# Optimization experiments

Measured on AMD Instinct MI355X. Metric: run time of the kernel, lower is better.

The kernel has to match this reference:

```python
import jax, jax.numpy as jnp
import numpy as np

L, N, E, D, H, B = 4, 50000, 800000, 128, 64, 16384
ED = 2 * D  # edge_dim
K = 7      # conv1d kernel size


def setup_inputs() -> dict:
    key = jax.random.key(0)
    ks = jax.random.split(key, 12)
    return {
        "x_nodes": jax.random.normal(ks[0], (L, N, 1), jnp.float32),
        "edge_index": jax.random.randint(ks[1], (L, 2, E), 0, N),
        "W1": jax.random.normal(ks[2], (L, 1, H), jnp.float32) * 0.1,
        "b1": jnp.zeros((L, H), jnp.float32),
        "gamma": jnp.ones((L, H), jnp.float32),
        "beta": jnp.zeros((L, H), jnp.float32),
        "W2": jax.random.normal(ks[3], (L, H, D), jnp.float32) * 0.05,
        "b2": jnp.zeros((L, D), jnp.float32),
        "conv_w": jax.random.normal(ks[4], (ED, ED, K), jnp.float32) * 0.02,
        "conv_b": jnp.zeros((ED,), jnp.float32),
        "lc_w": jax.random.normal(ks[5], (ED, L), jnp.float32) * 0.05,
        "lc_b": jnp.zeros((L,), jnp.float32),
        "link_w": jax.random.normal(ks[6], (ED, 2), jnp.float32) * 0.05,
        "link_b": jnp.zeros((2,), jnp.float32),
        "now_layer": jax.random.randint(ks[7], (B,), 0, L),
        "leftnode": jax.random.randint(ks[8], (B,), 0, N),
        "rightnode": jax.random.randint(ks[9], (B,), 0, N),
    }


def gcn_conv(x, src, dst, norm, W, b):
    # x: [N, Fin] -> [N, Fout]; symmetric-normalized message passing (GCNConv)
    xw = x @ W
    out = jax.ops.segment_sum(norm[:, None] * xw[src], dst, num_segments=N)
    return out + b


def gcn_layer(x, ei, W1, b1, g, bt, W2, b2):
    loops = jnp.arange(N, dtype=ei.dtype)
    src = jnp.concatenate([ei[0], loops])
    dst = jnp.concatenate([ei[1], loops])
    deg = jax.ops.segment_sum(jnp.ones_like(src, jnp.float32), dst, num_segments=N)
    dis = jax.lax.rsqrt(jnp.maximum(deg, 1e-12))
    norm = dis[src] * dis[dst]
    h = gcn_conv(x, src, dst, norm, W1, b1)
    # BatchNorm1d (training mode: batch stats over nodes)
    mu = h.mean(axis=0)
    var = h.var(axis=0)
    h = g * (h - mu) * jax.lax.rsqrt(var + 1e-5) + bt
    h = jax.nn.relu(h)
    return gcn_conv(h, src, dst, norm, W2, b2)


def reference(x_nodes, edge_index, W1, b1, gamma, beta, W2, b2,
              conv_w, conv_b, lc_w, lc_b, link_w, link_b,
              now_layer, leftnode, rightnode):
    # Per-layer GCN embeddings (fixed small L -> Python loop is fine, keeps peak memory low)
    embeds = jnp.stack([
        gcn_layer(x_nodes[i], edge_index[i], W1[i], b1[i], gamma[i], beta[i], W2[i], b2[i])
        for i in range(L)
    ])  # [L, N, D]

    # Edge features: gather per-sample layer-specific node embeddings and concat
    left = embeds[now_layer, leftnode]    # [B, D]
    right = embeds[now_layer, rightnode]  # [B, D]
    layer_specific = jnp.concatenate([left, right], axis=-1)  # [B, ED]

    # Conv1d applied unbatched on [ED, B] (convolves across batch dim, as in original)
    dn = jax.lax.conv_dimension_numbers((1, ED, B), (ED, ED, K), ('NCH', 'OIH', 'NCH'))
    y = jax.lax.conv_general_dilated(layer_specific.T[None], conv_w, (1,), [(3, 3)],
                                     dimension_numbers=dn)[0]  # [ED, B]
    shared = jax.nn.relu(y + conv_b[:, None]).T  # [B, ED]

    discriminant_outs = shared @ lc_w + lc_b  # [B, L]

    # Ortho_algorithm: remove shared component from specific, combine with shared
    dot = jnp.sum(layer_specific * shared, axis=-1, keepdims=True)
    nrm = jnp.sum(shared * shared, axis=-1, keepdims=True)
    enhanced = layer_specific - (dot / (nrm + 1e-12)) * shared + shared  # [B, ED]

    prediction_outs = enhanced @ link_w + link_b  # [B, 2]
    return prediction_outs, discriminant_outs
```

## Files before the change

kernel.cpp:

```cpp
#include <hip/hip_runtime.h>
#include <hip/hip_bf16.h>

#define Lc 4
#define Nc 50000
#define Ec 800000
#define Bc 16384
#define EDc 256
#define Kc 7
#define Mtot (Lc * Nc)
#define KDIM (EDc * Kc)

#define BINW 512
#define BSH 9
#define FB 98
#define NBINS (FB * Lc)
#define CAPc 12288
#define CHUNK 8192
#define FBLK ((Ec + CHUNK - 1) / CHUNK)

#define PADTOT 33024
#define PADBIT (1 << 24)

typedef __attribute__((ext_vector_type(8))) short bf16x8;
typedef __attribute__((ext_vector_type(4))) float f32x4;

static __device__ __forceinline__ unsigned short f2bf(float f) {
    unsigned u = __float_as_uint(f);
    unsigned r = (u + 0x7fffu + ((u >> 16) & 1u)) >> 16;
    return (unsigned short)r;
}
static __device__ __forceinline__ float bf2f(unsigned short u) {
    return __uint_as_float(((unsigned)u) << 16);
}


__global__ __launch_bounds__(1024) void k_binfill(const int* __restrict__ ei,
                                                  int* __restrict__ binCursor,
                                                  int* __restrict__ binned) {
    int l = blockIdx.y;
    int e0 = blockIdx.x * CHUNK;
    __shared__ int lh[FB], lcur[FB];
    if (threadIdx.x < FB) lh[threadIdx.x] = 0;
    __syncthreads();
    const int* srcp = ei + (size_t)l * 2 * Ec;
    const int* dstp = srcp + Ec;
#pragma unroll
    for (int it = 0; it < CHUNK / 1024; it++) {
        int idx = e0 + it * 1024 + threadIdx.x;
        if (idx < Ec) atomicAdd(&lh[dstp[idx] >> BSH], 1);
    }
    __syncthreads();
    if (threadIdx.x < FB) {
        int c = lh[threadIdx.x];
        int bin = l * FB + threadIdx.x;
        int st = c ? atomicAdd(&binCursor[bin], c) : 0;
        lcur[threadIdx.x] = bin * CAPc + min(st, CAPc);
        lh[threadIdx.x] = bin * CAPc + CAPc;
    }
    __syncthreads();
#pragma unroll
    for (int it = 0; it < CHUNK / 1024; it++) {
        int idx = e0 + it * 1024 + threadIdx.x;
        if (idx < Ec) {
            int d = dstp[idx], sv = srcp[idx];
            int t = d >> BSH;
            int pos = atomicAdd(&lcur[t], 1);
            if (pos < lh[t]) binned[pos] = (sv << BSH) | (d & (BINW - 1));
        }
    }
}

__global__ void k_mark(const int* __restrict__ now, const int* __restrict__ lnn,
                       const int* __restrict__ rnn, int* __restrict__ ord,
                       unsigned* __restrict__ bitmap, int* __restrict__ gcnt) {
    int b = blockIdx.x * 256 + threadIdx.x;
    for (int p = b; p < PADTOT; p += 16384) ord[p] = PADBIT;
    int l = now[b];
    int a1 = l * Nc + lnn[b];
    atomicOr(&bitmap[a1 >> 5], 1u << (a1 & 31));
    int a2 = l * Nc + rnn[b];
    atomicOr(&bitmap[a2 >> 5], 1u << (a2 & 31));
    int lane = threadIdx.x & 63;
#pragma unroll
    for (int ll = 0; ll < 4; ll++) {
        unsigned long long m = __ballot(l == ll);
        if (m && lane == __builtin_ctzll(m)) atomicAdd(&gcnt[ll], __popcll(m));
    }
}

__global__ void k_order2(const int* __restrict__ now, const int* __restrict__ gcnt,
                         int* __restrict__ gcur, int* __restrict__ ord) {
    int b = blockIdx.x * 256 + threadIdx.x;
    int l = now[b];
    int segBase = 0;
    for (int ll = 0; ll < l; ll++) segBase += (2 * gcnt[ll] + 63) & ~63;
    int lane = threadIdx.x & 63;
#pragma unroll
    for (int ll = 0; ll < 4; ll++) {
        unsigned long long m = __ballot(l == ll);
        if (!m) continue;
        int ldr = __builtin_ctzll(m);
        int bs = 0;
        if (lane == ldr) bs = atomicAdd(&gcur[ll], __popcll(m));
        bs = __shfl(bs, ldr);
        if (l == ll) {
            int rk = __popcll(m & (lane ? ((1ull << lane) - 1) : 0ull));
            int sp = segBase + 2 * (bs + rk);
            ord[sp] = (2 * b) | (ll << 20);
            ord[sp + 1] = (2 * b + 1) | (ll << 20);
        }
    }
}

__global__ __launch_bounds__(512) void k_csr(const int* __restrict__ binCnt,
                                             const int* __restrict__ binned,
                                             const float* __restrict__ x_nodes,
                                             const unsigned* __restrict__ bitmap,
                                             int* __restrict__ csr,
                                             int* __restrict__ rstart,
                                             int* __restrict__ cnt,
                                             float* __restrict__ dis,
                                             float* __restrict__ g) {
    int b = blockIdx.x;
    int l = b / FB, gg = b % FB;
    int rs = b * CAPc;
    int cntb = binCnt[b];
    if (cntb > CAPc) cntb = CAPc;
    int re = rs + cntb;
    __shared__ int hist[BINW];
    hist[threadIdx.x] = 0;
    __syncthreads();
    for (int i = rs + threadIdx.x; i < re; i += 512)
        atomicAdd(&hist[binned[i] & (BINW - 1)], 1);
    __syncthreads();
    int lane = threadIdx.x & 63, wid = threadIdx.x >> 6;
    int v = hist[threadIdx.x];
    int x = v;
#pragma unroll
    for (int off = 1; off < 64; off <<= 1) {
        int y = __shfl_up(x, off);
        if (lane >= off) x += y;
    }
    __shared__ int ws[8];
    if (lane == 63) ws[wid] = x;
    __syncthreads();
    int carry = 0;
    for (int w = 0; w < wid; w++) carry += ws[w];
    int exc = x - v + carry;
    int n = gg * BINW + threadIdx.x;
    int n4 = l * Nc + n;
    if (n < Nc) {
        rstart[n4] = rs + exc;
        cnt[n4] = v;
        float dn = rsqrtf((float)v + 1.0f);
        dis[n4] = dn;
        g[n4] = dn * x_nodes[(size_t)l * Nc + n];
    }
    __syncthreads();
    hist[threadIdx.x] = rs + exc;
    __syncthreads();
    int lbase = l * Nc + gg * BINW;
    for (int i = rs + threadIdx.x; i < re; i += 512) {
        unsigned p = (unsigned)binned[i];
        int d = p & (BINW - 1);
        int nn4 = lbase + d;
        if ((bitmap[nn4 >> 5] >> (nn4 & 31)) & 1u) {
            int pos = atomicAdd(&hist[d], 1);
            csr[pos] = (int)(p >> BSH);
        }
    }
}

__global__ __launch_bounds__(512) void k_s_bin(const int* __restrict__ binCnt,
                                               const int* __restrict__ binned,
                                               const float* __restrict__ g,
                                               const float* __restrict__ dis,
                                               float2* __restrict__ ns,
                                               double* __restrict__ stats) {
    int b = blockIdx.x;
    int l = b / FB, gg = b % FB;
    int rs = b * CAPc;
    int cntb = binCnt[b];
    if (cntb > CAPc) cntb = CAPc;
    int re = rs + cntb;
    const float* gl = g + (size_t)l * Nc;
    __shared__ float acc[BINW];
    acc[threadIdx.x] = 0.f;
    __syncthreads();
    for (int i = rs + threadIdx.x; i < re; i += 512) {
        unsigned p = (unsigned)binned[i];
        atomicAdd(&acc[p & (BINW - 1)], gl[p >> BSH]);
    }
    __syncthreads();
    int n = gg * BINW + threadIdx.x;
    int n4 = l * Nc + n;
    double v = 0.0, v2 = 0.0;
    if (n < Nc) {
        float dn = dis[n4];
        float sf = dn * (acc[threadIdx.x] + g[n4]);
        ns[n4] = make_float2(dn, sf);
        v = (double)sf;
        v2 = (double)sf * (double)sf;
    }
    for (int m = 32; m; m >>= 1) { v += __shfl_xor(v, m); v2 += __shfl_xor(v2, m); }
    __shared__ double r0[8], r1[8];
    int wid = threadIdx.x >> 6, lane = threadIdx.x & 63;
    if (lane == 0) { r0[wid] = v; r1[wid] = v2; }
    __syncthreads();
    if (threadIdx.x == 0) {
        double a = 0, bb = 0;
        for (int w = 0; w < 8; w++) { a += r0[w]; bb += r1[w]; }
        atomicAdd(&stats[l * 2 + 0], a);
        atomicAdd(&stats[l * 2 + 1], bb);
    }
}

__global__ void k_cvec4(const double* __restrict__ stats, const float* __restrict__ W1,
                        const float* __restrict__ gamma, float* __restrict__ cbuf) {
    int l = threadIdx.x >> 6, h = threadIdx.x & 63;
    double mean = stats[l * 2] / (double)Nc;
    double var = stats[l * 2 + 1] / (double)Nc - mean * mean;
    float w = W1[l * 64 + h];
    cbuf[l * 72 + h] = gamma[l * 64 + h] * w * rsqrtf((float)var * w * w + 1e-5f);
    if (h == 0) cbuf[l * 72 + 64] = (float)mean;
}


__global__ __launch_bounds__(256) void k_agg(const int* __restrict__ ord,
        const int* __restrict__ lnn, const int* __restrict__ rnn,
        const int* __restrict__ rstart, const int* __restrict__ cnt,
        const int* __restrict__ csr, const float2* __restrict__ ns,
        const float* __restrict__ cbuf, const float* __restrict__ beta,
        unsigned short* __restrict__ acch) {
    int pos = blockIdx.x * 4 + (threadIdx.x >> 6);
    int lane = threadIdx.x & 63;
    int ordv = ord[pos];
    if (ordv & PADBIT) { acch[(size_t)pos * 64 + lane] = 0; return; }
    int side = ordv & 0xFFFFF;
    int l = (ordv >> 20) & 3;
    int b = side >> 1;
    int n = (side & 1) ? rnn[b] : lnn[b];
    int n4 = l * Nc + n;
    float c = cbuf[l * 72 + lane], mu = cbuf[l * 72 + 64], bt = beta[l * 64 + lane];
    const float2* nsl = ns + (size_t)l * Nc;
    int st = rstart[n4], deg = cnt[n4];
    float a = 0.f;
    for (int base = 0; base < deg; base += 64) {
        int e = base + lane;
        int sv = (e < deg) ? csr[st + e] : 0;
        float nv = 0.f, fv = 0.f;
        if (e < deg) {
            float2 nf = nsl[sv];
            nv = nf.x; fv = nf.y;
        }
        int m = min(64, deg - base);
        for (int j = 0; j < m; j++) {
            float nj = __shfl(nv, j);
            float fj = __shfl(fv, j);
            a += nj * fmaxf(c * (fj - mu) + bt, 0.f);
        }
    }
    float2 nself = ns[n4];
    float hs = fmaxf(c * (nself.y - mu) + bt, 0.f);
    a = nself.x * a + nself.x * nself.x * hs;
    acch[(size_t)pos * 64 + lane] = f2bf(a);
}

__global__ __launch_bounds__(256) void k_embgemm(const unsigned short* __restrict__ acch,
        const int* __restrict__ ord, const unsigned short* __restrict__ w2t,
        const float* __restrict__ b2, unsigned short* __restrict__ lsh) {
    int t0 = blockIdx.x * 16;
    int wn = threadIdx.x >> 6, lane = threadIdx.x & 63;
    int lrow = lane & 15, lg = lane >> 4;
    int l = (ord[t0] >> 20) & 3;
    const unsigned short* ap = acch + (size_t)(t0 + lrow) * 64 + lg * 8;
    const unsigned short* bp = w2t + (size_t)(l * 128 + wn * 32 + lrow) * 64 + lg * 8;
    f32x4 acc[2] = {};
#pragma unroll
    for (int kt = 0; kt < 2; kt++) {
        bf16x8 a = *(const bf16x8*)(ap + kt * 32);
        bf16x8 b0 = *(const bf16x8*)(bp + kt * 32);
        bf16x8 b1 = *(const bf16x8*)(bp + 16 * 64 + kt * 32);
        acc[0] = __builtin_amdgcn_mfma_f32_16x16x32_bf16(a, b0, acc[0], 0, 0, 0);
        acc[1] = __builtin_amdgcn_mfma_f32_16x16x32_bf16(a, b1, acc[1], 0, 0, 0);
    }
#pragma unroll
    for (int r = 0; r < 4; r++) {
        int pos = t0 + lg * 4 + r;
        int ordv = ord[pos];
        if (ordv & PADBIT) continue;
        int side = ordv & 0xFFFFF;
        size_t base = (size_t)(side >> 1) * 256 + (side & 1) * 128;
#pragma unroll
        for (int ni = 0; ni < 2; ni++) {
            int n = wn * 32 + ni * 16 + lrow;
            lsh[base + n] = f2bf(acc[ni][r] + b2[l * 128 + n]);
        }
    }
}


__global__ void k_wbf(const float* __restrict__ w, unsigned short* __restrict__ wbt) {
    int i = blockIdx.x * 256 + threadIdx.x;
    int co = i / KDIM;
    int r = i % KDIM;
    int ci = r / Kc, k = r % Kc;
    wbt[(size_t)co * KDIM + k * EDc + ci] = f2bf(w[i]);
}

__global__ void k_w2t(const float* __restrict__ W2, unsigned short* __restrict__ w2t,
                      int* __restrict__ zeroRegion, int zn) {
    int i = blockIdx.x * 256 + threadIdx.x;
    if (i < zn) zeroRegion[i] = 0;
    int l = i >> 13, r = i & 8191;
    int d = r >> 6, h = r & 63;
    w2t[i] = f2bf(W2[(size_t)(l * 64 + h) * 128 + d]);
}

__global__ __launch_bounds__(512, 1) void k_convmma(const unsigned short* __restrict__ lsh,
                                                    const unsigned short* __restrict__ wbt,
                                                    const float* __restrict__ cb,
                                                    float* __restrict__ sh) {
    __shared__ unsigned short lsa[70 * EDc];
    int b0 = blockIdx.x * 64;
    int wid = threadIdx.x >> 6, lane = threadIdx.x & 63;
    int lrow = lane & 15, lg = lane >> 4;

    for (int idx = threadIdx.x; idx < 70 * 32; idx += 512) {
        int r = idx >> 5, c = idx & 31;
        int grow = b0 - 3 + r;
        uint4 v = make_uint4(0u, 0u, 0u, 0u);
        if ((unsigned)grow < (unsigned)Bc)
            v = *(const uint4*)(lsh + (size_t)grow * EDc + c * 8);
        int byte = (r * 512 + c * 16) ^ ((r & 7) << 4);
        *(uint4*)((char*)lsa + byte) = v;
    }
    __syncthreads();

    const unsigned short* w0 = wbt + (size_t)(wid * 32 + lrow) * KDIM + lg * 8;

    f32x4 acc[4][2] = {};
    bf16x8 br0[8][2], br1[8][2];

#pragma unroll
    for (int tt = 0; tt < 8; tt++)
#pragma unroll
        for (int ni = 0; ni < 2; ni++)
            br0[tt][ni] = *(const bf16x8*)(w0 + ni * 16 * KDIM + tt * 32);

#pragma unroll
    for (int k = 0; k < Kc; k++) {
        if (k < Kc - 1) {
#pragma unroll
            for (int tt = 0; tt < 8; tt++)
#pragma unroll
                for (int ni = 0; ni < 2; ni++) {
                    bf16x8 v = *(const bf16x8*)(w0 + ni * 16 * KDIM + (k + 1) * 256 + tt * 32);
                    if (k & 1) br0[tt][ni] = v; else br1[tt][ni] = v;
                }
        }
#pragma unroll
        for (int tt = 0; tt < 8; tt++) {
            bf16x8 a[4];
#pragma unroll
            for (int mi = 0; mi < 4; mi++) {
                int l = mi * 16 + lrow + k;
                a[mi] = *(const bf16x8*)((const char*)lsa + l * 512
                        + ((lg * 16 + tt * 64) ^ ((l & 7) << 4)));
            }
#pragma unroll
            for (int mi = 0; mi < 4; mi++)
#pragma unroll
                for (int ni = 0; ni < 2; ni++) {
                    bf16x8 bv = (k & 1) ? br1[tt][ni] : br0[tt][ni];
                    acc[mi][ni] = __builtin_amdgcn_mfma_f32_16x16x32_bf16(
                        a[mi], bv, acc[mi][ni], 0, 0, 0);
                }
        }
    }

#pragma unroll
    for (int mi = 0; mi < 4; mi++) {
        int rbase = b0 + mi * 16 + lg * 4;
#pragma unroll
        for (int ni = 0; ni < 2; ni++) {
            int co = wid * 32 + ni * 16 + lrow;
            float bias = cb[co];
#pragma unroll
            for (int r = 0; r < 4; r++)
                sh[(size_t)(rbase + r) * EDc + co] = fmaxf(acc[mi][ni][r] + bias, 0.0f);
        }
    }
}

__global__ __launch_bounds__(256) void k_final(const unsigned short* __restrict__ lsh,
                        const float* __restrict__ sh,
                        const float* __restrict__ lc_w, const float* __restrict__ lc_b,
                        const float* __restrict__ link_w, const float* __restrict__ link_b,
                        float* __restrict__ out) {
    int b = blockIdx.x * 4 + (threadIdx.x >> 6);
    int lane = threadIdx.x & 63;
    float lsv[4], shv[4];
    float dot = 0.f, nrm = 0.f;
#pragma unroll
    for (int i = 0; i < 4; i++) {
        int ci = lane + i * 64;
        lsv[i] = bf2f(lsh[(size_t)b * 256 + ci]);
        shv[i] = sh[(size_t)b * 256 + ci];
        dot += lsv[i] * shv[i];
        nrm += shv[i] * shv[i];
    }
    for (int m = 32; m; m >>= 1) { dot += __shfl_xor(dot, m); nrm += __shfl_xor(nrm, m); }
    float coef = dot / (nrm + 1e-12f);
    float p0 = 0.f, p1 = 0.f, d0 = 0.f, d1 = 0.f, d2 = 0.f, d3 = 0.f;
#pragma unroll
    for (int i = 0; i < 4; i++) {
        int ci = lane + i * 64;
        float e = lsv[i] - coef * shv[i] + shv[i];
        p0 += e * link_w[ci * 2];
        p1 += e * link_w[ci * 2 + 1];
        d0 += shv[i] * lc_w[ci * 4];
        d1 += shv[i] * lc_w[ci * 4 + 1];
        d2 += shv[i] * lc_w[ci * 4 + 2];
        d3 += shv[i] * lc_w[ci * 4 + 3];
    }
    for (int m = 32; m; m >>= 1) {
        p0 += __shfl_xor(p0, m); p1 += __shfl_xor(p1, m);
        d0 += __shfl_xor(d0, m); d1 += __shfl_xor(d1, m);
        d2 += __shfl_xor(d2, m); d3 += __shfl_xor(d3, m);
    }
    if (lane == 0) {
        out[b * 2]     = p0 + link_b[0];
        out[b * 2 + 1] = p1 + link_b[1];
        float* dd = out + 2 * Bc;
        dd[b * 4]     = d0 + lc_b[0];
        dd[b * 4 + 1] = d1 + lc_b[1];
        dd[b * 4 + 2] = d2 + lc_b[2];
        dd[b * 4 + 3] = d3 + lc_b[3];
    }
}


extern "C" void kernel_launch(void* const* d_in, const int* in_sizes, int n_in,
                              void* d_out, int out_size, void* d_ws, size_t ws_size,
                              hipStream_t stream) {
    const float* x_nodes    = (const float*)d_in[0];
    const int*   edge_index = (const int*)d_in[1];
    const float* W1   = (const float*)d_in[2];
    const float* gamma = (const float*)d_in[4];
    const float* beta  = (const float*)d_in[5];
    const float* W2   = (const float*)d_in[6];
    const float* b2   = (const float*)d_in[7];
    const float* conv_w = (const float*)d_in[8];
    const float* conv_b = (const float*)d_in[9];
    const float* lc_w   = (const float*)d_in[10];
    const float* lc_b   = (const float*)d_in[11];
    const float* link_w = (const float*)d_in[12];
    const float* link_b = (const float*)d_in[13];
    const int* now = (const int*)d_in[14];
    const int* ln  = (const int*)d_in[15];
    const int* rn  = (const int*)d_in[16];
    float* out = (float*)d_out;

    char* base = (char*)d_ws;
    size_t off = 0;
    auto carve = [&](size_t bytes) {
        void* p = base + off;
        off = (off + bytes + 255) & ~(size_t)255;
        return p;
    };
    int*      binCursor = (int*)carve(NBINS * 4);
    int*      gcnt      = (int*)carve(4 * 4);
    int*      gcur      = (int*)carve(4 * 4);
    unsigned* bitmap    = (unsigned*)carve(6272 * 4);
    double*   stats     = (double*)carve(8 * 8);
    int*    binned    = (int*)carve((size_t)NBINS * CAPc * 4);
    int*    rstart    = (int*)carve((size_t)Mtot * 4);
    int*    cnt       = (int*)carve((size_t)Mtot * 4);
    int*    csr       = (int*)carve((size_t)NBINS * CAPc * 4);
    float*  dis       = (float*)carve((size_t)Mtot * 4);
    float*  g         = (float*)carve((size_t)Mtot * 4);
    float2* ns        = (float2*)carve((size_t)Mtot * 8);
    float*  cbuf      = (float*)carve(Lc * 72 * 4);
    int*    ord       = (int*)carve((size_t)PADTOT * 4);
    unsigned short* acch = (unsigned short*)carve((size_t)PADTOT * 64 * 2);
    float*  shb       = (float*)carve((size_t)Bc * 256 * 4);
    unsigned short* lsh = (unsigned short*)carve((size_t)Bc * 256 * 2);
    unsigned short* wbt = (unsigned short*)carve((size_t)EDc * KDIM * 2);
    unsigned short* w2t = (unsigned short*)carve((size_t)Lc * 128 * 64 * 2);
    (void)ws_size;

    int zn = (int)(((char*)(stats + 8) - (char*)binCursor) / 4);

    k_w2t<<<128, 256, 0, stream>>>(W2, w2t, binCursor, zn);
    k_wbf<<<1792, 256, 0, stream>>>(conv_w, wbt);
    k_mark<<<64, 256, 0, stream>>>(now, ln, rn, ord, bitmap, gcnt);

    k_binfill<<<dim3(FBLK, Lc), 1024, 0, stream>>>(edge_index, binCursor, binned);
    k_csr<<<NBINS, 512, 0, stream>>>(binCursor, binned, x_nodes, bitmap,
                                     csr, rstart, cnt, dis, g);
    k_s_bin<<<NBINS, 512, 0, stream>>>(binCursor, binned, g, dis, ns, stats);
    k_cvec4<<<1, 256, 0, stream>>>(stats, W1, gamma, cbuf);
    k_order2<<<64, 256, 0, stream>>>(now, gcnt, gcur, ord);
    k_agg<<<PADTOT / 4, 256, 0, stream>>>(ord, ln, rn, rstart, cnt, csr, ns,
                                          cbuf, beta, acch);
    k_embgemm<<<PADTOT / 16, 256, 0, stream>>>(acch, ord, w2t, b2, lsh);

    k_convmma<<<Bc / 64, 512, 0, stream>>>(lsh, wbt, conv_b, shb);
    k_final<<<Bc / 4, 256, 0, stream>>>(lsh, shb, lc_w, lc_b, link_w, link_b, out);
}
```

Baseline: 179.0 us.

## Fuse conv with final head, drop global bin atomics, merge small kernels

The conv MMA kernel now keeps the ReLU'd shared features in LDS and computes the orthogonal projection and both output heads in-block. This removes the 16 MB fp32 round trip through global memory and one launch. Edge binning now writes into per-block fixed-capacity segments (SCAP = 160) with no global cursor atomics. The CSR and sum kernels therefore scan padded segments, which adds slot checks and can drop edges if a block's bin overflows. The weight-prep kernels are merged, and the order and BN-coefficient kernels are merged, to cut launch count.

After: 184.8 us. +3.2%, slower.

```diff
diff --git a/kernel.cpp b/kernel.cpp
--- a/kernel.cpp
+++ b/kernel.cpp
@@ -16,7 +16,8 @@
 #define NBINS (FB * Lc)
 #define CAPc 12288
 #define CHUNK 8192
-#define FBLK ((Ec + CHUNK - 1) / CHUNK)
+#define FBLK 98
+#define SCAP 160
 
 #define PADTOT 33024
 #define PADBIT (1 << 24)
@@ -34,39 +35,22 @@
 }
 
 
-__global__ __launch_bounds__(1024) void k_binfill(const int* __restrict__ ei,
-                                                  int* __restrict__ binCursor,
-                                                  int* __restrict__ binned) {
-    int l = blockIdx.y;
-    int e0 = blockIdx.x * CHUNK;
-    __shared__ int lh[FB], lcur[FB];
-    if (threadIdx.x < FB) lh[threadIdx.x] = 0;
-    __syncthreads();
-    const int* srcp = ei + (size_t)l * 2 * Ec;
-    const int* dstp = srcp + Ec;
-#pragma unroll
-    for (int it = 0; it < CHUNK / 1024; it++) {
-        int idx = e0 + it * 1024 + threadIdx.x;
-        if (idx < Ec) atomicAdd(&lh[dstp[idx] >> BSH], 1);
-    }
-    __syncthreads();
-    if (threadIdx.x < FB) {
-        int c = lh[threadIdx.x];
-        int bin = l * FB + threadIdx.x;
-        int st = c ? atomicAdd(&binCursor[bin], c) : 0;
-        lcur[threadIdx.x] = bin * CAPc + min(st, CAPc);
-        lh[threadIdx.x] = bin * CAPc + CAPc;
-    }
-    __syncthreads();
-#pragma unroll
-    for (int it = 0; it < CHUNK / 1024; it++) {
-        int idx = e0 + it * 1024 + threadIdx.x;
-        if (idx < Ec) {
-            int d = dstp[idx], sv = srcp[idx];
-            int t = d >> BSH;
-            int pos = atomicAdd(&lcur[t], 1);
-            if (pos < lh[t]) binned[pos] = (sv << BSH) | (d & (BINW - 1));
-        }
+__global__ void k_prep(const float* __restrict__ conv_w, unsigned short* __restrict__ wbt,
+                       const float* __restrict__ W2, unsigned short* __restrict__ w2t,
+                       int* __restrict__ zeroRegion, int zn) {
+    int bb = blockIdx.x;
+    if (bb < 1792) {
+        int i = bb * 256 + threadIdx.x;
+        int co = i / KDIM;
+        int r = i % KDIM;
+        int ci = r / Kc, k = r % Kc;
+        wbt[(size_t)co * KDIM + k * EDc + ci] = f2bf(conv_w[i]);
+    } else {
+        int i = (bb - 1792) * 256 + threadIdx.x;
+        if (i < zn) zeroRegion[i] = 0;
+        int l = i >> 13, r = i & 8191;
+        int d = r >> 6, h = r & 63;
+        w2t[i] = f2bf(W2[(size_t)(l * 64 + h) * 128 + d]);
     }
 }
 
@@ -88,8 +72,162 @@
     }
 }
 
-__global__ void k_order2(const int* __restrict__ now, const int* __restrict__ gcnt,
-                         int* __restrict__ gcur, int* __restrict__ ord) {
+
+__global__ __launch_bounds__(512) void k_binfill(const int* __restrict__ ei,
+                                                 int* __restrict__ blkCnt,
+                                                 int* __restrict__ binned) {
+    int l = blockIdx.y, bx = blockIdx.x;
+    int e0 = bx * CHUNK;
+    __shared__ int lcur[FB];
+    if (threadIdx.x < FB) lcur[threadIdx.x] = 0;
+    __syncthreads();
+    const int* srcp = ei + (size_t)l * 2 * Ec;
+    const int* dstp = srcp + Ec;
+    int segBase = (l * FBLK + bx) * FB;
+#pragma unroll
+    for (int it = 0; it < CHUNK / 512; it++) {
+        int idx = e0 + it * 512 + threadIdx.x;
+        if (idx < Ec) {
+            int d = dstp[idx], sv = srcp[idx];
+            int t = d >> BSH;
+            int slot = atomicAdd(&lcur[t], 1);
+            if (slot < SCAP)
+                binned[(size_t)(segBase + t) * SCAP + slot] = (sv << BSH) | (d & (BINW - 1));
+        }
+    }
+    __syncthreads();
+    if (threadIdx.x < FB) blkCnt[segBase + threadIdx.x] = min(lcur[threadIdx.x], SCAP);
+}
+
+__global__ __launch_bounds__(512) void k_csr(const int* __restrict__ blkCnt,
+                                             const int* __restrict__ binned,
+                                             const float* __restrict__ x_nodes,
+                                             const unsigned* __restrict__ bitmap,
+                                             int* __restrict__ csr,
+                                             int* __restrict__ rstart,
+                                             int* __restrict__ cnt,
+                                             float* __restrict__ dis,
+                                             float* __restrict__ g) {
+    int b = blockIdx.x;
+    int l = b / FB, gg = b % FB;
+    int rs = b * CAPc;
+    __shared__ int segc[FBLK];
+    __shared__ int hist[BINW];
+    if (threadIdx.x < FBLK) segc[threadIdx.x] = blkCnt[(l * FBLK + threadIdx.x) * FB + gg];
+    hist[threadIdx.x] = 0;
+    __syncthreads();
+    const int PADN = FBLK * SCAP;
+    size_t binBase = (size_t)l * FBLK * FB + gg;
+    for (int i = threadIdx.x; i < PADN; i += 512) {
+        int seg = i / SCAP, sl = i - seg * SCAP;
+        if (sl < segc[seg]) {
+            int p = binned[(binBase + (size_t)seg * FB) * SCAP + sl];
+            atomicAdd(&hist[p & (BINW - 1)], 1);
+        }
+    }
+    __syncthreads();
+    int lane = threadIdx.x & 63, wid = threadIdx.x >> 6;
+    int v = hist[threadIdx.x];
+    int x = v;
+#pragma unroll
+    for (int off = 1; off < 64; off <<= 1) {
+        int y = __shfl_up(x, off);
+        if (lane >= off) x += y;
+    }
+    __shared__ int ws[8];
+    if (lane == 63) ws[wid] = x;
+    __syncthreads();
+    int carry = 0;
+    for (int w = 0; w < wid; w++) carry += ws[w];
+    int exc = x - v + carry;
+    int n = gg * BINW + threadIdx.x;
+    int n4 = l * Nc + n;
+    if (n < Nc) {
+        rstart[n4] = rs + exc;
+        cnt[n4] = v;
+        float dn = rsqrtf((float)v + 1.0f);
+        dis[n4] = dn;
+        g[n4] = dn * x_nodes[(size_t)l * Nc + n];
+    }
+    __syncthreads();
+    hist[threadIdx.x] = rs + exc;
+    __syncthreads();
+    int lbase = l * Nc + gg * BINW;
+    for (int i = threadIdx.x; i < PADN; i += 512) {
+        int seg = i / SCAP, sl = i - seg * SCAP;
+        if (sl < segc[seg]) {
+            unsigned p = (unsigned)binned[(binBase + (size_t)seg * FB) * SCAP + sl];
+            int d = p & (BINW - 1);
+            int nn4 = lbase + d;
+            if ((bitmap[nn4 >> 5] >> (nn4 & 31)) & 1u) {
+                int pos = atomicAdd(&hist[d], 1);
+                csr[pos] = (int)(p >> BSH);
+            }
+        }
+    }
+}
+
+__global__ __launch_bounds__(512) void k_s_bin(const int* __restrict__ blkCnt,
+                                               const int* __restrict__ binned,
+                                               const float* __restrict__ g,
+                                               const float* __restrict__ dis,
+                                               float2* __restrict__ ns,
+                                               double* __restrict__ stats) {
+    int b = blockIdx.x;
+    int l = b / FB, gg = b % FB;
+    const float* gl = g + (size_t)l * Nc;
+    __shared__ int segc[FBLK];
+    __shared__ float acc[BINW];
+    if (threadIdx.x < FBLK) segc[threadIdx.x] = blkCnt[(l * FBLK + threadIdx.x) * FB + gg];
+    acc[threadIdx.x] = 0.f;
+    __syncthreads();
+    const int PADN = FBLK * SCAP;
+    size_t binBase = (size_t)l * FBLK * FB + gg;
+    for (int i = threadIdx.x; i < PADN; i += 512) {
+        int seg = i / SCAP, sl = i - seg * SCAP;
+        if (sl < segc[seg]) {
+            unsigned p = (unsigned)binned[(binBase + (size_t)seg * FB) * SCAP + sl];
+            atomicAdd(&acc[p & (BINW - 1)], gl[p >> BSH]);
+        }
+    }
+    __syncthreads();
+    int n = gg * BINW + threadIdx.x;
+    int n4 = l * Nc + n;
+    double v = 0.0, v2 = 0.0;
+    if (n < Nc) {
+        float dn = dis[n4];
+        float sf = dn * (acc[threadIdx.x] + g[n4]);
+        ns[n4] = make_float2(dn, sf);
+        v = (double)sf;
+        v2 = (double)sf * (double)sf;
+    }
+    for (int m = 32; m; m >>= 1) { v += __shfl_xor(v, m); v2 += __shfl_xor(v2, m); }
+    __shared__ double r0[8], r1[8];
+    int wid = threadIdx.x >> 6, lane = threadIdx.x & 63;
+    if (lane == 0) { r0[wid] = v; r1[wid] = v2; }
+    __syncthreads();
+    if (threadIdx.x == 0) {
+        double a = 0, bb = 0;
+        for (int w = 0; w < 8; w++) { a += r0[w]; bb += r1[w]; }
+        atomicAdd(&stats[l * 2 + 0], a);
+        atomicAdd(&stats[l * 2 + 1], bb);
+    }
+}
+
+
+__global__ __launch_bounds__(256) void k_ordcvec(const int* __restrict__ now,
+        const int* __restrict__ gcnt, int* __restrict__ gcur, int* __restrict__ ord,
+        const double* __restrict__ stats, const float* __restrict__ W1,
+        const float* __restrict__ gamma, float* __restrict__ cbuf) {
+    if (blockIdx.x == 64) {
+        int l = threadIdx.x >> 6, h = threadIdx.x & 63;
+        double mean = stats[l * 2] / (double)Nc;
+        double var = stats[l * 2 + 1] / (double)Nc - mean * mean;
+        float w = W1[l * 64 + h];
+        cbuf[l * 72 + h] = gamma[l * 64 + h] * w * rsqrtf((float)var * w * w + 1e-5f);
+        if (h == 0) cbuf[l * 72 + 64] = (float)mean;
+        return;
+    }
     int b = blockIdx.x * 256 + threadIdx.x;
     int l = now[b];
     int segBase = 0;
@@ -110,119 +248,6 @@
             ord[sp + 1] = (2 * b + 1) | (ll << 20);
         }
     }
-}
-
-__global__ __launch_bounds__(512) void k_csr(const int* __restrict__ binCnt,
-                                             const int* __restrict__ binned,
-                                             const float* __restrict__ x_nodes,
-                                             const unsigned* __restrict__ bitmap,
-                                             int* __restrict__ csr,
-                                             int* __restrict__ rstart,
-                                             int* __restrict__ cnt,
-                                             float* __restrict__ dis,
-                                             float* __restrict__ g) {
-    int b = blockIdx.x;
-    int l = b / FB, gg = b % FB;
-    int rs = b * CAPc;
-    int cntb = binCnt[b];
-    if (cntb > CAPc) cntb = CAPc;
-    int re = rs + cntb;
-    __shared__ int hist[BINW];
-    hist[threadIdx.x] = 0;
-    __syncthreads();
-    for (int i = rs + threadIdx.x; i < re; i += 512)
-        atomicAdd(&hist[binned[i] & (BINW - 1)], 1);
-    __syncthreads();
-    int lane = threadIdx.x & 63, wid = threadIdx.x >> 6;
-    int v = hist[threadIdx.x];
-    int x = v;
-#pragma unroll
-    for (int off = 1; off < 64; off <<= 1) {
-        int y = __shfl_up(x, off);
-        if (lane >= off) x += y;
-    }
-    __shared__ int ws[8];
-    if (lane == 63) ws[wid] = x;
-    __syncthreads();
-    int carry = 0;
-    for (int w = 0; w < wid; w++) carry += ws[w];
-    int exc = x - v + carry;
-    int n = gg * BINW + threadIdx.x;
-    int n4 = l * Nc + n;
-    if (n < Nc) {
-        rstart[n4] = rs + exc;
-        cnt[n4] = v;
-        float dn = rsqrtf((float)v + 1.0f);
-        dis[n4] = dn;
-        g[n4] = dn * x_nodes[(size_t)l * Nc + n];
-    }
-    __syncthreads();
-    hist[threadIdx.x] = rs + exc;
-    __syncthreads();
-    int lbase = l * Nc + gg * BINW;
-    for (int i = rs + threadIdx.x; i < re; i += 512) {
-        unsigned p = (unsigned)binned[i];
-        int d = p & (BINW - 1);
-        int nn4 = lbase + d;
-        if ((bitmap[nn4 >> 5] >> (nn4 & 31)) & 1u) {
-            int pos = atomicAdd(&hist[d], 1);
-            csr[pos] = (int)(p >> BSH);
-        }
-    }
-}
-
-__global__ __launch_bounds__(512) void k_s_bin(const int* __restrict__ binCnt,
-                                               const int* __restrict__ binned,
-                                               const float* __restrict__ g,
-                                               const float* __restrict__ dis,
-                                               float2* __restrict__ ns,
-                                               double* __restrict__ stats) {
-    int b = blockIdx.x;
-    int l = b / FB, gg = b % FB;
-    int rs = b * CAPc;
-    int cntb = binCnt[b];
-    if (cntb > CAPc) cntb = CAPc;
-    int re = rs + cntb;
-    const float* gl = g + (size_t)l * Nc;
-    __shared__ float acc[BINW];
-    acc[threadIdx.x] = 0.f;
-    __syncthreads();
-    for (int i = rs + threadIdx.x; i < re; i += 512) {
-        unsigned p = (unsigned)binned[i];
-        atomicAdd(&acc[p & (BINW - 1)], gl[p >> BSH]);
-    }
-    __syncthreads();
-    int n = gg * BINW + threadIdx.x;
-    int n4 = l * Nc + n;
-    double v = 0.0, v2 = 0.0;
-    if (n < Nc) {
-        float dn = dis[n4];
-        float sf = dn * (acc[threadIdx.x] + g[n4]);
-        ns[n4] = make_float2(dn, sf);
-        v = (double)sf;
-        v2 = (double)sf * (double)sf;
-    }
-    for (int m = 32; m; m >>= 1) { v += __shfl_xor(v, m); v2 += __shfl_xor(v2, m); }
-    __shared__ double r0[8], r1[8];
-    int wid = threadIdx.x >> 6, lane = threadIdx.x & 63;
-    if (lane == 0) { r0[wid] = v; r1[wid] = v2; }
-    __syncthreads();
-    if (threadIdx.x == 0) {
-        double a = 0, bb = 0;
-        for (int w = 0; w < 8; w++) { a += r0[w]; bb += r1[w]; }
-        atomicAdd(&stats[l * 2 + 0], a);
-        atomicAdd(&stats[l * 2 + 1], bb);
-    }
-}
-
-__global__ void k_cvec4(const double* __restrict__ stats, const float* __restrict__ W1,
-                        const float* __restrict__ gamma, float* __restrict__ cbuf) {
-    int l = threadIdx.x >> 6, h = threadIdx.x & 63;
-    double mean = stats[l * 2] / (double)Nc;
-    double var = stats[l * 2 + 1] / (double)Nc - mean * mean;
-    float w = W1[l * 64 + h];
-    cbuf[l * 72 + h] = gamma[l * 64 + h] * w * rsqrtf((float)var * w * w + 1e-5f);
-    if (h == 0) cbuf[l * 72 + 64] = (float)mean;
 }
 
 
@@ -300,28 +325,13 @@
 }
 
 
-__global__ void k_wbf(const float* __restrict__ w, unsigned short* __restrict__ wbt) {
-    int i = blockIdx.x * 256 + threadIdx.x;
-    int co = i / KDIM;
-    int r = i % KDIM;
-    int ci = r / Kc, k = r % Kc;
-    wbt[(size_t)co * KDIM + k * EDc + ci] = f2bf(w[i]);
-}
-
-__global__ void k_w2t(const float* __restrict__ W2, unsigned short* __restrict__ w2t,
-                      int* __restrict__ zeroRegion, int zn) {
-    int i = blockIdx.x * 256 + threadIdx.x;
-    if (i < zn) zeroRegion[i] = 0;
-    int l = i >> 13, r = i & 8191;
-    int d = r >> 6, h = r & 63;
-    w2t[i] = f2bf(W2[(size_t)(l * 64 + h) * 128 + d]);
-}
-
-__global__ __launch_bounds__(512, 1) void k_convmma(const unsigned short* __restrict__ lsh,
-                                                    const unsigned short* __restrict__ wbt,
-                                                    const float* __restrict__ cb,
-                                                    float* __restrict__ sh) {
+__global__ __launch_bounds__(512, 1) void k_convfinal(const unsigned short* __restrict__ lsh,
+        const unsigned short* __restrict__ wbt, const float* __restrict__ cb,
+        const float* __restrict__ lc_w, const float* __restrict__ lc_b,
+        const float* __restrict__ link_w, const float* __restrict__ link_b,
+        float* __restrict__ out) {
     __shared__ unsigned short lsa[70 * EDc];
+    __shared__ float shs[64][EDc];
     int b0 = blockIdx.x * 64;
     int wid = threadIdx.x >> 6, lane = threadIdx.x & 63;
     int lrow = lane & 15, lg = lane >> 4;
@@ -381,62 +391,61 @@
 
 #pragma unroll
     for (int mi = 0; mi < 4; mi++) {
-        int rbase = b0 + mi * 16 + lg * 4;
+        int rrow = mi * 16 + lg * 4;
 #pragma unroll
         for (int ni = 0; ni < 2; ni++) {
             int co = wid * 32 + ni * 16 + lrow;
             float bias = cb[co];
 #pragma unroll
             for (int r = 0; r < 4; r++)
-                sh[(size_t)(rbase + r) * EDc + co] = fmaxf(acc[mi][ni][r] + bias, 0.0f);
-        }
-    }
-}
-
-__global__ __launch_bounds__(256) void k_final(const unsigned short* __restrict__ lsh,
-                        const float* __restrict__ sh,
-                        const float* __restrict__ lc_w, const float* __restrict__ lc_b,
-                        const float* __restrict__ link_w, const float* __restrict__ link_b,
-                        float* __restrict__ out) {
-    int b = blockIdx.x * 4 + (threadIdx.x >> 6);
-    int lane = threadIdx.x & 63;
-    float lsv[4], shv[4];
-    float dot = 0.f, nrm = 0.f;
-#pragma unroll
-    for (int i = 0; i < 4; i++) {
-        int ci = lane + i * 64;
-        lsv[i] = bf2f(lsh[(size_t)b * 256 + ci]);
-        shv[i] = sh[(size_t)b * 256 + ci];
-        dot += lsv[i] * shv[i];
-        nrm += shv[i] * shv[i];
-    }
-    for (int m = 32; m; m >>= 1) { dot += __shfl_xor(dot, m); nrm += __shfl_xor(nrm, m); }
-    float coef = dot / (nrm + 1e-12f);
-    float p0 = 0.f, p1 = 0.f, d0 = 0.f, d1 = 0.f, d2 = 0.f, d3 = 0.f;
-#pragma unroll
-    for (int i = 0; i < 4; i++) {
-        int ci = lane + i * 64;
-        float e = lsv[i] - coef * shv[i] + shv[i];
-        p0 += e * link_w[ci * 2];
-        p1 += e * link_w[ci * 2 + 1];
-        d0 += shv[i] * lc_w[ci * 4];
-        d1 += shv[i] * lc_w[ci * 4 + 1];
-        d2 += shv[i] * lc_w[ci * 4 + 2];
-        d3 += shv[i] * lc_w[ci * 4 + 3];
-    }
-    for (int m = 32; m; m >>= 1) {
-        p0 += __shfl_xor(p0, m); p1 += __shfl_xor(p1, m);
-        d0 += __shfl_xor(d0, m); d1 += __shfl_xor(d1, m);
-        d2 += __shfl_xor(d2, m); d3 += __shfl_xor(d3, m);
-    }
-    if (lane == 0) {
-        out[b * 2]     = p0 + link_b[0];
-        out[b * 2 + 1] = p1 + link_b[1];
-        float* dd = out + 2 * Bc;
-        dd[b * 4]     = d0 + lc_b[0];
-        dd[b * 4 + 1] = d1 + lc_b[1];
-        dd[b * 4 + 2] = d2 + lc_b[2];
-        dd[b * 4 + 3] = d3 + lc_b[3];
+                shs[rrow + r][co] = fmaxf(acc[mi][ni][r] + bias, 0.0f);
+        }
+    }
+    __syncthreads();
+
+    for (int rr = 0; rr < 8; rr++) {
+        int row = wid * 8 + rr;
+        int b = b0 + row;
+        int lr = row + 3;
+        int swz = (lr & 7) << 4;
+        float lsv[4], shv[4];
+        float dot = 0.f, nrm = 0.f;
+#pragma unroll
+        for (int i = 0; i < 4; i++) {
+            int ci = lane + i * 64;
+            lsv[i] = bf2f(*(const unsigned short*)((const char*)lsa + lr * 512 + ((ci * 2) ^ swz)));
+            shv[i] = shs[row][ci];
+            dot += lsv[i] * shv[i];
+            nrm += shv[i] * shv[i];
+        }
+        for (int m = 32; m; m >>= 1) { dot += __shfl_xor(dot, m); nrm += __shfl_xor(nrm, m); }
+        float coef = dot / (nrm + 1e-12f);
+        float p0 = 0.f, p1 = 0.f, d0 = 0.f, d1 = 0.f, d2 = 0.f, d3 = 0.f;
+#pragma unroll
+        for (int i = 0; i < 4; i++) {
+            int ci = lane + i * 64;
+            float e = lsv[i] - coef * shv[i] + shv[i];
+            p0 += e * link_w[ci * 2];
+            p1 += e * link_w[ci * 2 + 1];
+            d0 += shv[i] * lc_w[ci * 4];
+            d1 += shv[i] * lc_w[ci * 4 + 1];
+            d2 += shv[i] * lc_w[ci * 4 + 2];
+            d3 += shv[i] * lc_w[ci * 4 + 3];
+        }
+        for (int m = 32; m; m >>= 1) {
+            p0 += __shfl_xor(p0, m); p1 += __shfl_xor(p1, m);
+            d0 += __shfl_xor(d0, m); d1 += __shfl_xor(d1, m);
+            d2 += __shfl_xor(d2, m); d3 += __shfl_xor(d3, m);
+        }
+        if (lane == 0) {
+            out[b * 2]     = p0 + link_b[0];
+            out[b * 2 + 1] = p1 + link_b[1];
+            float* dd = out + 2 * Bc;
+            dd[b * 4]     = d0 + lc_b[0];
+            dd[b * 4 + 1] = d1 + lc_b[1];
+            dd[b * 4 + 2] = d2 + lc_b[2];
+            dd[b * 4 + 3] = d3 + lc_b[3];
+        }
     }
 }
 
@@ -469,43 +478,38 @@
         off = (off + bytes + 255) & ~(size_t)255;
         return p;
     };
-    int*      binCursor = (int*)carve(NBINS * 4);
-    int*      gcnt      = (int*)carve(4 * 4);
-    int*      gcur      = (int*)carve(4 * 4);
-    unsigned* bitmap    = (unsigned*)carve(6272 * 4);
-    double*   stats     = (double*)carve(8 * 8);
-    int*    binned    = (int*)carve((size_t)NBINS * CAPc * 4);
-    int*    rstart    = (int*)carve((size_t)Mtot * 4);
-    int*    cnt       = (int*)carve((size_t)Mtot * 4);
-    int*    csr       = (int*)carve((size_t)NBINS * CAPc * 4);
-    float*  dis       = (float*)carve((size_t)Mtot * 4);
-    float*  g         = (float*)carve((size_t)Mtot * 4);
-    float2* ns        = (float2*)carve((size_t)Mtot * 8);
-    float*  cbuf      = (float*)carve(Lc * 72 * 4);
-    int*    ord       = (int*)carve((size_t)PADTOT * 4);
+    unsigned* bitmap = (unsigned*)carve(6272 * 4);
+    int*      gcnt   = (int*)carve(4 * 4);
+    int*      gcur   = (int*)carve(4 * 4);
+    double*   stats  = (double*)carve(8 * 8);
+    int*    blkCnt   = (int*)carve((size_t)Lc * FBLK * FB * 4);
+    int*    binned   = (int*)carve((size_t)Lc * FBLK * FB * SCAP * 4);
+    int*    rstart   = (int*)carve((size_t)Mtot * 4);
+    int*    cnt      = (int*)carve((size_t)Mtot * 4);
+    int*    csr      = (int*)carve((size_t)NBINS * CAPc * 4);
+    float*  dis      = (float*)carve((size_t)Mtot * 4);
+    float*  g        = (float*)carve((size_t)Mtot * 4);
+    float2* ns       = (float2*)carve((size_t)Mtot * 8);
+    float*  cbuf     = (float*)carve(Lc * 72 * 4);
+    int*    ord      = (int*)carve((size_t)PADTOT * 4);
     unsigned short* acch = (unsigned short*)carve((size_t)PADTOT * 64 * 2);
-    float*  shb       = (float*)carve((size_t)Bc * 256 * 4);
-    unsigned short* lsh = (unsigned short*)carve((size_t)Bc * 256 * 2);
-    unsigned short* wbt = (unsigned short*)carve((size_t)EDc * KDIM * 2);
-    unsigned short* w2t = (unsigned short*)carve((size_t)Lc * 128 * 64 * 2);
+    unsigned short* lsh  = (unsigned short*)carve((size_t)Bc * 256 * 2);
+    unsigned short* wbt  = (unsigned short*)carve((size_t)EDc * KDIM * 2);
+    unsigned short* w2t  = (unsigned short*)carve((size_t)Lc * 128 * 64 * 2);
     (void)ws_size;
 
-    int zn = (int)(((char*)(stats + 8) - (char*)binCursor) / 4);
-
-    k_w2t<<<128, 256, 0, stream>>>(W2, w2t, binCursor, zn);
-    k_wbf<<<1792, 256, 0, stream>>>(conv_w, wbt);
+    int zn = (int)(((char*)(stats + 8) - (char*)bitmap) / 4);
+
+    k_prep<<<1920, 256, 0, stream>>>(conv_w, wbt, W2, w2t, (int*)bitmap, zn);
     k_mark<<<64, 256, 0, stream>>>(now, ln, rn, ord, bitmap, gcnt);
-
-    k_binfill<<<dim3(FBLK, Lc), 1024, 0, stream>>>(edge_index, binCursor, binned);
-    k_csr<<<NBINS, 512, 0, stream>>>(binCursor, binned, x_nodes, bitmap,
+    k_binfill<<<dim3(FBLK, Lc), 512, 0, stream>>>(edge_index, blkCnt, binned);
+    k_csr<<<NBINS, 512, 0, stream>>>(blkCnt, binned, x_nodes, bitmap,
                                      csr, rstart, cnt, dis, g);
-    k_s_bin<<<NBINS, 512, 0, stream>>>(binCursor, binned, g, dis, ns, stats);
-    k_cvec4<<<1, 256, 0, stream>>>(stats, W1, gamma, cbuf);
-    k_order2<<<64, 256, 0, stream>>>(now, gcnt, gcur, ord);
+    k_s_bin<<<NBINS, 512, 0, stream>>>(blkCnt, binned, g, dis, ns, stats);
+    k_ordcvec<<<65, 256, 0, stream>>>(now, gcnt, gcur, ord, stats, W1, gamma, cbuf);
     k_agg<<<PADTOT / 4, 256, 0, stream>>>(ord, ln, rn, rstart, cnt, csr, ns,
                                           cbuf, beta, acch);
     k_embgemm<<<PADTOT / 16, 256, 0, stream>>>(acch, ord, w2t, b2, lsh);
-
-    k_convmma<<<Bc / 64, 512, 0, stream>>>(lsh, wbt, conv_b, shb);
-    k_final<<<Bc / 4, 256, 0, stream>>>(lsh, shb, lc_w, lc_b, link_w, link_b, out);
-}
+    k_convfinal<<<Bc / 64, 512, 0, stream>>>(lsh, wbt, conv_b,
+                                             lc_w, lc_b, link_w, link_b, out);
+}
```
